# Kernel tuning notes

Measured on AMD Instinct MI355X. Metric: run time of the kernel, lower is better.

The kernel has to match this reference:

```python
import jax, jax.numpy as jnp
import numpy as np

B, S, D, H = 2, 4096, 256, 8
P = 64               # proj_dim_l
R = S // P           # proj_dim_r = 64, P*R == S
DH = D // H          # head_dim = 32


def setup_inputs() -> dict:
    key = jax.random.key(0)
    kx, kl, kr, kv, ko = jax.random.split(key, 5)
    scale = 0.05  # stand-in for xavier-uniform scale
    x  = jax.random.normal(kx, (B, S, D), dtype=jnp.float32)
    Wl = jax.random.normal(kl, (D, P), dtype=jnp.float32) * scale
    Wr = jax.random.normal(kr, (D, R), dtype=jnp.float32) * scale
    Wv = jax.random.normal(kv, (D, D), dtype=jnp.float32) * scale
    Wo = jax.random.normal(ko, (D, D), dtype=jnp.float32) * scale
    return {"x": x, "Wl": Wl, "Wr": Wr, "Wv": Wv, "Wo": Wo}


def reference(x, Wl, Wr, Wv, Wo):
    b, s, d = x.shape
    # value projection + head split -> (b, H, S, DH). Dropout p=0 (eval) = identity.
    v = (x @ Wv).reshape(b, s, H, DH).transpose(0, 2, 1, 3)
    # factorized score: row n is vec(outer(l_n, r_n)) of length P*R == S
    l = x @ Wl                                   # (b, S, P)
    r = x @ Wr                                   # (b, S, R)
    attn = (l[:, :, :, None] * r[:, :, None, :]).reshape(b, s, s)  # (b, S, S)
    score = jax.nn.softmax(attn, axis=-1)        # (b, S, S)
    # shared score across heads, per-head value matmul
    o = jnp.einsum('bnm,bhmd->bhnd', score, v)   # (b, H, S, DH)
    o = o.transpose(0, 2, 1, 3).reshape(b, s, d) # concat heads
    return o @ Wo
```

## Files before the change

### kernel.cpp

```cpp
#include <hip/hip_runtime.h>
#include <hip/hip_bf16.h>

typedef __attribute__((ext_vector_type(8))) __bf16 bf16x8;
typedef __attribute__((ext_vector_type(4))) __bf16 bf16x4;
typedef __attribute__((ext_vector_type(4))) float  f32x4;

#define MFMA16(a, b, c) __builtin_amdgcn_mfma_f32_16x16x32_bf16((a), (b), (c), 0, 0, 0)

static constexpr size_t OFF_WVT  = 0;
static constexpr size_t OFF_WLT  = OFF_WVT + 256 * 256 * 2;
static constexpr size_t OFF_WRT  = OFF_WLT + 64 * 256 * 2;
static constexpr size_t OFF_WOT  = OFF_WRT + 64 * 256 * 2;
static constexpr size_t OFF_VT   = 1u << 20;
static constexpr size_t OFF_L    = 6u << 20;
static constexpr size_t OFF_R    = 8u << 20;
static constexpr size_t OFF_PART = 10u << 20;
static constexpr size_t OFF_ZP   = 26u << 20;

__device__ __forceinline__ float fast_exp2(float x) {
  float e;
  asm("v_exp_f32 %0, %1" : "=v"(e) : "v"(x));
  return e;
}

__device__ __forceinline__ bf16x8 cvt8(float4 a, float4 b) {
  bf16x8 o;
  o[0] = (__bf16)a.x; o[1] = (__bf16)a.y; o[2] = (__bf16)a.z; o[3] = (__bf16)a.w;
  o[4] = (__bf16)b.x; o[5] = (__bf16)b.y; o[6] = (__bf16)b.z; o[7] = (__bf16)b.w;
  return o;
}

__global__ __launch_bounds__(256) void k_prepw(const float* __restrict__ Wv,
                                               const float* __restrict__ Wl,
                                               const float* __restrict__ Wr,
                                               const float* __restrict__ Wo,
                                               __bf16* __restrict__ Wvt,
                                               __bf16* __restrict__ Wlt,
                                               __bf16* __restrict__ Wrt,
                                               __bf16* __restrict__ Wot) {
  const int idx = blockIdx.x * 256 + threadIdx.x;
  if (idx < 65536) {
    const int k = idx >> 8, n = idx & 255;
    Wvt[n * 256 + k] = (__bf16)Wv[idx];
  } else if (idx < 81920) {
    const int j = idx - 65536;
    const int k = j >> 6, n = j & 63;
    Wlt[n * 256 + k] = (__bf16)Wl[j];
  } else if (idx < 98304) {
    const int j = idx - 81920;
    const int k = j >> 6, n = j & 63;
    Wrt[n * 256 + k] = (__bf16)Wr[j];
  } else {
    const int j = idx - 98304;
    const int k = j >> 8, n = j & 255;
    Wot[n * 256 + k] = (__bf16)Wo[j];
  }
}

__global__ __launch_bounds__(256) void k_proj(const float* __restrict__ x,
                                              const __bf16* __restrict__ Wvt,
                                              const __bf16* __restrict__ Wlt,
                                              const __bf16* __restrict__ Wrt,
                                              __bf16* __restrict__ Vt,
                                              float* __restrict__ lbuf,
                                              float* __restrict__ rbuf) {
  __shared__ __align__(16) __bf16 vs[8 * 64 * 8];
  const int t = threadIdx.x;
  const int lane = t & 63, wave = t >> 6;
  const int l16 = lane & 15, quad = lane >> 4;
  const int wr = wave >> 1, wc = wave & 1;
  const int rbk = blockIdx.x;
  const int ct  = blockIdx.y;
  const __bf16* Wt;
  int colbase;
  if (ct < 4)       { Wt = Wvt; colbase = ct * 64; }
  else if (ct == 4) { Wt = Wlt; colbase = 0; }
  else              { Wt = Wrt; colbase = 0; }
  const int row0 = rbk * 64 + wr * 32;
  const int c0   = colbase + wc * 32;
  f32x4 acc[2][2] = {};
  for (int kk = 0; kk < 256; kk += 32) {
    const int ko = kk + quad * 8;
    const float* xr0 = x + (size_t)(row0 + l16) * 256 + ko;
    const float* xr1 = x + (size_t)(row0 + 16 + l16) * 256 + ko;
    bf16x8 a0 = cvt8(*(const float4*)xr0, *(const float4*)(xr0 + 4));
    bf16x8 a1 = cvt8(*(const float4*)xr1, *(const float4*)(xr1 + 4));
    bf16x8 b0 = *(const bf16x8*)(Wt + (size_t)(c0 + l16) * 256 + ko);
    bf16x8 b1 = *(const bf16x8*)(Wt + (size_t)(c0 + 16 + l16) * 256 + ko);
    acc[0][0] = MFMA16(a0, b0, acc[0][0]);
    acc[0][1] = MFMA16(a0, b1, acc[0][1]);
    acc[1][0] = MFMA16(a1, b0, acc[1][0]);
    acc[1][1] = MFMA16(a1, b1, acc[1][1]);
  }
  if (ct < 4) {
#pragma unroll
    for (int mt = 0; mt < 2; ++mt)
#pragma unroll
      for (int nt = 0; nt < 2; ++nt) {
        const int m8 = wr * 4 + mt * 2 + (quad >> 1);
        const int d  = wc * 32 + nt * 16 + l16;
        bf16x4 o;
        o.x = (__bf16)acc[mt][nt][0];
        o.y = (__bf16)acc[mt][nt][1];
        o.z = (__bf16)acc[mt][nt][2];
        o.w = (__bf16)acc[mt][nt][3];
        *(bf16x4*)(&vs[m8 * 512 + d * 8 + (quad & 1) * 4]) = o;
      }
    __syncthreads();
    const int m8 = t >> 5, s32 = t & 31;
    const int bat = rbk >> 6, mc = rbk & 63;
    bf16x8 a = *(const bf16x8*)(&vs[m8 * 512 + s32 * 16]);
    bf16x8 b = *(const bf16x8*)(&vs[m8 * 512 + s32 * 16 + 8]);
    __bf16* dst = Vt + (size_t)bat * 1048576 + (size_t)mc * 16384 +
                  m8 * 2048 + ct * 512 + s32 * 16;
    *(bf16x8*)dst       = a;
    *(bf16x8*)(dst + 8) = b;
  } else {
    float* dstb = (ct == 4) ? lbuf : rbuf;
#pragma unroll
    for (int mt = 0; mt < 2; ++mt)
#pragma unroll
      for (int nt = 0; nt < 2; ++nt) {
        const int col = c0 + nt * 16 + l16;
        const int gr  = rbk * 64 + wr * 32 + mt * 16 + quad * 4;
#pragma unroll
        for (int rr = 0; rr < 4; ++rr)
          dstb[(size_t)(gr + rr) * 64 + col] = acc[mt][nt][rr];
      }
  }
}

__global__ __launch_bounds__(512, 2) void k_attn(const float* __restrict__ lbuf,
                                                 const float* __restrict__ rbuf,
                                                 const __bf16* __restrict__ Vt,
                                                 __bf16* __restrict__ part,
                                                 float* __restrict__ zpart) {
  __shared__ __align__(16) char smem[74240];
  __bf16* vt0 = (__bf16*)smem;
  __bf16* vt1 = (__bf16*)(smem + 32768);
  float*  ls  = (float*)(smem + 65536);
  const int t = threadIdx.x;
  const int lane = t & 63, w = t >> 6;
  const int l16 = lane & 15, quad = lane >> 4;
  const int wr = w >> 1, wc = w & 1;
  const int rb = blockIdx.x;
  const int sp = blockIdx.y;
  const int g0 = rb * 128;
  const int bat = rb >> 5;
  const __bf16* Vbase = Vt + (size_t)bat * 1048576;
  const int ck0 = sp * 16;

  {
    const int idx = t * 4;
    const int row = idx >> 4, c = idx & 15;
    f32x4 v = *(const f32x4*)(lbuf + (size_t)(g0 + row) * 64 + ck0 + c);
    ls[row * 17 + c + 0] = v[0];
    ls[row * 17 + c + 1] = v[1];
    ls[row * 17 + c + 2] = v[2];
    ls[row * 17 + c + 3] = v[3];
  }
  const float LOG2E = 1.44269504088896f;
  float rreg[2][16];
#pragma unroll
  for (int mt = 0; mt < 2; ++mt) {
    const float* rp = rbuf + (size_t)(g0 + wr * 32 + mt * 16 + l16) * 64;
    f32x4 a = *(const f32x4*)(rp + quad * 8);
    f32x4 b = *(const f32x4*)(rp + quad * 8 + 4);
    f32x4 c = *(const f32x4*)(rp + 32 + quad * 8);
    f32x4 d = *(const f32x4*)(rp + 32 + quad * 8 + 4);
#pragma unroll
    for (int j = 0; j < 4; ++j) {
      rreg[mt][j]      = a[j] * LOG2E;
      rreg[mt][4 + j]  = b[j] * LOG2E;
      rreg[mt][8 + j]  = c[j] * LOG2E;
      rreg[mt][12 + j] = d[j] * LOG2E;
    }
  }

  f32x4 acc[2][8] = {};
  float zacc[2] = {0.f, 0.f};
  bf16x8 stg[4];

  {
    const __bf16* src = Vbase + (size_t)ck0 * 16384;
#pragma unroll
    for (int i = 0; i < 4; ++i) stg[i] = *(const bf16x8*)(src + (size_t)(i * 512 + t) * 8);
#pragma unroll
    for (int i = 0; i < 4; ++i) *(bf16x8*)(vt0 + (i * 512 + t) * 8) = stg[i];
  }
  __syncthreads();

  for (int kc = 0; kc < 16; ++kc) {
    __bf16* cur = (kc & 1) ? vt1 : vt0;
    __bf16* nxt = (kc & 1) ? vt0 : vt1;
    if (kc < 15) {
      const __bf16* src = Vbase + (size_t)(ck0 + kc + 1) * 16384;
#pragma unroll
      for (int i = 0; i < 4; ++i) stg[i] = *(const bf16x8*)(src + (size_t)(i * 512 + t) * 8);
    }
    bf16x8 af[2][2];
#pragma unroll
    for (int mt = 0; mt < 2; ++mt) {
      const float lv = ls[(wr * 32 + mt * 16 + l16) * 17 + kc];
#pragma unroll
      for (int kk = 0; kk < 2; ++kk)
#pragma unroll
        for (int j = 0; j < 8; ++j) {
          const float e = fast_exp2(lv * rreg[mt][kk * 8 + j]);
          zacc[mt] += e;
          af[mt][kk][j] = (__bf16)e;
        }
    }
#pragma unroll
    for (int kk = 0; kk < 2; ++kk)
#pragma unroll
      for (int nt = 0; nt < 8; ++nt) {
        bf16x8 bv = *(const bf16x8*)(cur + (kk * 4 + quad) * 2048 +
                                     (wc * 128 + nt * 16 + l16) * 8);
        acc[0][nt] = MFMA16(af[0][kk], bv, acc[0][nt]);
        acc[1][nt] = MFMA16(af[1][kk], bv, acc[1][nt]);
      }
    if (kc < 15) {
#pragma unroll
      for (int i = 0; i < 4; ++i) *(bf16x8*)(nxt + (i * 512 + t) * 8) = stg[i];
    }
    __syncthreads();
  }

#pragma unroll
  for (int mt = 0; mt < 2; ++mt) {
    float z = zacc[mt];
    z += __shfl_xor(z, 16);
    z += __shfl_xor(z, 32);
    if (wc == 0 && quad == 0)
      zpart[(size_t)sp * 8192 + g0 + wr * 32 + mt * 16 + l16] = z;
  }

  __bf16* ctile = (__bf16*)smem;
#pragma unroll
  for (int mt = 0; mt < 2; ++mt)
#pragma unroll
    for (int nt = 0; nt < 8; ++nt) {
      const int r0 = wr * 32 + mt * 16 + quad * 4;
      const int c  = wc * 128 + nt * 16 + l16;
#pragma unroll
      for (int rr = 0; rr < 4; ++rr)
        ctile[(r0 + rr) * 264 + c] = (__bf16)acc[mt][nt][rr];
    }
  __syncthreads();
  __bf16* pb = part + (size_t)sp * (8192 * 256);
#pragma unroll
  for (int p = 0; p < 8; ++p) {
    const int u = p * 512 + t;
    const int row = u >> 5, seg = u & 31;
    *(bf16x8*)(pb + (size_t)(g0 + row) * 256 + seg * 8) =
        *(const bf16x8*)(ctile + row * 264 + seg * 8);
  }
}

__global__ __launch_bounds__(256) void k_outfix(const __bf16* __restrict__ part,
                                                const float* __restrict__ zpart,
                                                const __bf16* __restrict__ Wot,
                                                float* __restrict__ out) {
  const int t = threadIdx.x;
  const int lane = t & 63, w = t >> 6;
  const int l16 = lane & 15, quad = lane >> 4;
  const int wr = w >> 1, wc = w & 1;
  const int rb = blockIdx.x;
  const int arow = rb * 32 + wr * 16 + l16;
  float z = 0.f;
#pragma unroll
  for (int s = 0; s < 4; ++s) z += zpart[(size_t)s * 8192 + arow];
  const float iz = 1.0f / z;
  f32x4 acc[8] = {};
#pragma unroll 2
  for (int ks = 0; ks < 8; ++ks) {
    const int k0 = ks * 32 + quad * 8;
    float sum[8] = {};
#pragma unroll
    for (int s = 0; s < 4; ++s) {
      bf16x8 p = *(const bf16x8*)(part + (size_t)s * (8192 * 256) + (size_t)arow * 256 + k0);
#pragma unroll
      for (int j = 0; j < 8; ++j) sum[j] += (float)p[j];
    }
    bf16x8 afr;
#pragma unroll
    for (int j = 0; j < 8; ++j) afr[j] = (__bf16)(sum[j] * iz);
#pragma unroll
    for (int nt = 0; nt < 8; ++nt) {
      bf16x8 bv = *(const bf16x8*)(Wot + (size_t)(wc * 128 + nt * 16 + l16) * 256 + k0);
      acc[nt] = MFMA16(afr, bv, acc[nt]);
    }
  }
#pragma unroll
  for (int nt = 0; nt < 8; ++nt) {
    const int col = wc * 128 + nt * 16 + l16;
    const int r0  = rb * 32 + wr * 16 + quad * 4;
#pragma unroll
    for (int rr = 0; rr < 4; ++rr)
      out[(size_t)(r0 + rr) * 256 + col] = acc[nt][rr];
  }
}

extern "C" void kernel_launch(void* const* d_in, const int* in_sizes, int n_in,
                              void* d_out, int out_size, void* d_ws, size_t ws_size,
                              hipStream_t stream) {
  const float* x  = (const float*)d_in[0];
  const float* Wl = (const float*)d_in[1];
  const float* Wr = (const float*)d_in[2];
  const float* Wv = (const float*)d_in[3];
  const float* Wo = (const float*)d_in[4];
  char* ws = (char*)d_ws;
  __bf16* Wvt = (__bf16*)(ws + OFF_WVT);
  __bf16* Wlt = (__bf16*)(ws + OFF_WLT);
  __bf16* Wrt = (__bf16*)(ws + OFF_WRT);
  __bf16* Wot = (__bf16*)(ws + OFF_WOT);
  __bf16* Vt  = (__bf16*)(ws + OFF_VT);
  float*  lb  = (float*)(ws + OFF_L);
  float*  rbf = (float*)(ws + OFF_R);
  __bf16* prt = (__bf16*)(ws + OFF_PART);
  float*  zp  = (float*)(ws + OFF_ZP);
  float*  out = (float*)d_out;

  k_prepw<<<640, 256, 0, stream>>>(Wv, Wl, Wr, Wo, Wvt, Wlt, Wrt, Wot);
  k_proj<<<dim3(128, 6), 256, 0, stream>>>(x, Wvt, Wlt, Wrt, Vt, lb, rbf);
  k_attn<<<dim3(64, 4), 512, 0, stream>>>(lb, rbf, Vt, prt, zp);
  k_outfix<<<256, 256, 0, stream>>>(prt, zp, Wot, out);
}
```

Baseline: 136.2 us.

## Fuse weight prep into projection kernel and retile attention waves to 2x4

Removes the separate weight-conversion kernel. Each projection block now converts its own weight slice from fp32 into a transposed bf16 tile in shared memory, and the Wo transpose is spread across the l/r projection blocks. The attention kernel's wave layout changes from 4x2 to 2x4, so each wave handles 64 rows by 64 columns and every V fragment read from LDS feeds four MFMAs instead of two. This saves one launch and some global traffic, at the cost of redundant weight conversion in every block and higher register pressure in the attention kernel.

```diff
diff --git a/kernel.cpp b/kernel.cpp
--- a/kernel.cpp
+++ b/kernel.cpp
@@ -7,10 +7,7 @@
 
 #define MFMA16(a, b, c) __builtin_amdgcn_mfma_f32_16x16x32_bf16((a), (b), (c), 0, 0, 0)
 
-static constexpr size_t OFF_WVT  = 0;
-static constexpr size_t OFF_WLT  = OFF_WVT + 256 * 256 * 2;
-static constexpr size_t OFF_WRT  = OFF_WLT + 64 * 256 * 2;
-static constexpr size_t OFF_WOT  = OFF_WRT + 64 * 256 * 2;
+static constexpr size_t OFF_WOT  = 0;
 static constexpr size_t OFF_VT   = 1u << 20;
 static constexpr size_t OFF_L    = 6u << 20;
 static constexpr size_t OFF_R    = 8u << 20;
@@ -30,40 +27,16 @@
   return o;
 }
 
-__global__ __launch_bounds__(256) void k_prepw(const float* __restrict__ Wv,
-                                               const float* __restrict__ Wl,
-                                               const float* __restrict__ Wr,
-                                               const float* __restrict__ Wo,
-                                               __bf16* __restrict__ Wvt,
-                                               __bf16* __restrict__ Wlt,
-                                               __bf16* __restrict__ Wrt,
-                                               __bf16* __restrict__ Wot) {
-  const int idx = blockIdx.x * 256 + threadIdx.x;
-  if (idx < 65536) {
-    const int k = idx >> 8, n = idx & 255;
-    Wvt[n * 256 + k] = (__bf16)Wv[idx];
-  } else if (idx < 81920) {
-    const int j = idx - 65536;
-    const int k = j >> 6, n = j & 63;
-    Wlt[n * 256 + k] = (__bf16)Wl[j];
-  } else if (idx < 98304) {
-    const int j = idx - 81920;
-    const int k = j >> 6, n = j & 63;
-    Wrt[n * 256 + k] = (__bf16)Wr[j];
-  } else {
-    const int j = idx - 98304;
-    const int k = j >> 8, n = j & 255;
-    Wot[n * 256 + k] = (__bf16)Wo[j];
-  }
-}
-
 __global__ __launch_bounds__(256) void k_proj(const float* __restrict__ x,
-                                              const __bf16* __restrict__ Wvt,
-                                              const __bf16* __restrict__ Wlt,
-                                              const __bf16* __restrict__ Wrt,
+                                              const float* __restrict__ Wv,
+                                              const float* __restrict__ Wl,
+                                              const float* __restrict__ Wr,
+                                              const float* __restrict__ Wo,
                                               __bf16* __restrict__ Vt,
                                               float* __restrict__ lbuf,
-                                              float* __restrict__ rbuf) {
+                                              float* __restrict__ rbuf,
+                                              __bf16* __restrict__ Wot) {
+  __shared__ __align__(16) __bf16 wt[64 * 264];
   __shared__ __align__(16) __bf16 vs[8 * 64 * 8];
   const int t = threadIdx.x;
   const int lane = t & 63, wave = t >> 6;
@@ -71,13 +44,35 @@
   const int wr = wave >> 1, wc = wave & 1;
   const int rbk = blockIdx.x;
   const int ct  = blockIdx.y;
-  const __bf16* Wt;
-  int colbase;
-  if (ct < 4)       { Wt = Wvt; colbase = ct * 64; }
-  else if (ct == 4) { Wt = Wlt; colbase = 0; }
-  else              { Wt = Wrt; colbase = 0; }
+  const float* Wsrc;
+  int wstride, colbase;
+  if (ct < 4)       { Wsrc = Wv; wstride = 256; colbase = ct * 64; }
+  else if (ct == 4) { Wsrc = Wl; wstride = 64;  colbase = 0; }
+  else              { Wsrc = Wr; wstride = 64;  colbase = 0; }
+
+  if (ct >= 4) {
+    const int j = ((ct - 4) * 128 + rbk) * 256 + t;
+    const int k = j >> 8, n = j & 255;
+    Wot[n * 256 + k] = (__bf16)Wo[j];
+  }
+
+  {
+    const int kr = t >> 4;
+    const int n4 = (t & 15) * 4;
+#pragma unroll
+    for (int kk = 0; kk < 16; ++kk) {
+      const int k = kk * 16 + kr;
+      float4 v = *(const float4*)(Wsrc + (size_t)k * wstride + colbase + n4);
+      wt[(n4 + 0) * 264 + k] = (__bf16)v.x;
+      wt[(n4 + 1) * 264 + k] = (__bf16)v.y;
+      wt[(n4 + 2) * 264 + k] = (__bf16)v.z;
+      wt[(n4 + 3) * 264 + k] = (__bf16)v.w;
+    }
+  }
+  __syncthreads();
+
   const int row0 = rbk * 64 + wr * 32;
-  const int c0   = colbase + wc * 32;
+  const int c0l  = wc * 32;
   f32x4 acc[2][2] = {};
   for (int kk = 0; kk < 256; kk += 32) {
     const int ko = kk + quad * 8;
@@ -85,8 +80,8 @@
     const float* xr1 = x + (size_t)(row0 + 16 + l16) * 256 + ko;
     bf16x8 a0 = cvt8(*(const float4*)xr0, *(const float4*)(xr0 + 4));
     bf16x8 a1 = cvt8(*(const float4*)xr1, *(const float4*)(xr1 + 4));
-    bf16x8 b0 = *(const bf16x8*)(Wt + (size_t)(c0 + l16) * 256 + ko);
-    bf16x8 b1 = *(const bf16x8*)(Wt + (size_t)(c0 + 16 + l16) * 256 + ko);
+    bf16x8 b0 = *(const bf16x8*)(wt + (c0l + l16) * 264 + ko);
+    bf16x8 b1 = *(const bf16x8*)(wt + (c0l + 16 + l16) * 264 + ko);
     acc[0][0] = MFMA16(a0, b0, acc[0][0]);
     acc[0][1] = MFMA16(a0, b1, acc[0][1]);
     acc[1][0] = MFMA16(a1, b0, acc[1][0]);
@@ -121,7 +116,7 @@
     for (int mt = 0; mt < 2; ++mt)
 #pragma unroll
       for (int nt = 0; nt < 2; ++nt) {
-        const int col = c0 + nt * 16 + l16;
+        const int col = c0l + nt * 16 + l16;
         const int gr  = rbk * 64 + wr * 32 + mt * 16 + quad * 4;
 #pragma unroll
         for (int rr = 0; rr < 4; ++rr)
@@ -142,7 +137,7 @@
   const int t = threadIdx.x;
   const int lane = t & 63, w = t >> 6;
   const int l16 = lane & 15, quad = lane >> 4;
-  const int wr = w >> 1, wc = w & 1;
+  const int wr = w >> 2, wc = w & 3;
   const int rb = blockIdx.x;
   const int sp = blockIdx.y;
   const int g0 = rb * 128;
@@ -160,10 +155,10 @@
     ls[row * 17 + c + 3] = v[3];
   }
   const float LOG2E = 1.44269504088896f;
-  float rreg[2][16];
-#pragma unroll
-  for (int mt = 0; mt < 2; ++mt) {
-    const float* rp = rbuf + (size_t)(g0 + wr * 32 + mt * 16 + l16) * 64;
+  float rreg[4][16];
+#pragma unroll
+  for (int mt = 0; mt < 4; ++mt) {
+    const float* rp = rbuf + (size_t)(g0 + wr * 64 + mt * 16 + l16) * 64;
     f32x4 a = *(const f32x4*)(rp + quad * 8);
     f32x4 b = *(const f32x4*)(rp + quad * 8 + 4);
     f32x4 c = *(const f32x4*)(rp + 32 + quad * 8);
@@ -177,8 +172,8 @@
     }
   }
 
-  f32x4 acc[2][8] = {};
-  float zacc[2] = {0.f, 0.f};
+  f32x4 acc[4][4] = {};
+  float zacc[4] = {0.f, 0.f, 0.f, 0.f};
   bf16x8 stg[4];
 
   {
@@ -198,10 +193,10 @@
 #pragma unroll
       for (int i = 0; i < 4; ++i) stg[i] = *(const bf16x8*)(src + (size_t)(i * 512 + t) * 8);
     }
-    bf16x8 af[2][2];
-#pragma unroll
-    for (int mt = 0; mt < 2; ++mt) {
-      const float lv = ls[(wr * 32 + mt * 16 + l16) * 17 + kc];
+    bf16x8 af[4][2];
+#pragma unroll
+    for (int mt = 0; mt < 4; ++mt) {
+      const float lv = ls[(wr * 64 + mt * 16 + l16) * 17 + kc];
 #pragma unroll
       for (int kk = 0; kk < 2; ++kk)
 #pragma unroll
@@ -214,11 +209,13 @@
 #pragma unroll
     for (int kk = 0; kk < 2; ++kk)
 #pragma unroll
-      for (int nt = 0; nt < 8; ++nt) {
+      for (int nt = 0; nt < 4; ++nt) {
         bf16x8 bv = *(const bf16x8*)(cur + (kk * 4 + quad) * 2048 +
-                                     (wc * 128 + nt * 16 + l16) * 8);
+                                     (wc * 64 + nt * 16 + l16) * 8);
         acc[0][nt] = MFMA16(af[0][kk], bv, acc[0][nt]);
         acc[1][nt] = MFMA16(af[1][kk], bv, acc[1][nt]);
+        acc[2][nt] = MFMA16(af[2][kk], bv, acc[2][nt]);
+        acc[3][nt] = MFMA16(af[3][kk], bv, acc[3][nt]);
       }
     if (kc < 15) {
 #pragma unroll
@@ -228,21 +225,21 @@
   }
 
 #pragma unroll
-  for (int mt = 0; mt < 2; ++mt) {
+  for (int mt = 0; mt < 4; ++mt) {
     float z = zacc[mt];
     z += __shfl_xor(z, 16);
     z += __shfl_xor(z, 32);
     if (wc == 0 && quad == 0)
-      zpart[(size_t)sp * 8192 + g0 + wr * 32 + mt * 16 + l16] = z;
+      zpart[(size_t)sp * 8192 + g0 + wr * 64 + mt * 16 + l16] = z;
   }
 
   __bf16* ctile = (__bf16*)smem;
 #pragma unroll
-  for (int mt = 0; mt < 2; ++mt)
-#pragma unroll
-    for (int nt = 0; nt < 8; ++nt) {
-      const int r0 = wr * 32 + mt * 16 + quad * 4;
-      const int c  = wc * 128 + nt * 16 + l16;
+  for (int mt = 0; mt < 4; ++mt)
+#pragma unroll
+    for (int nt = 0; nt < 4; ++nt) {
+      const int r0 = wr * 64 + mt * 16 + quad * 4;
+      const int c  = wc * 64 + nt * 16 + l16;
 #pragma unroll
       for (int rr = 0; rr < 4; ++rr)
         ctile[(r0 + rr) * 264 + c] = (__bf16)acc[mt][nt][rr];
@@ -311,9 +308,6 @@
   const float* Wv = (const float*)d_in[3];
   const float* Wo = (const float*)d_in[4];
   char* ws = (char*)d_ws;
-  __bf16* Wvt = (__bf16*)(ws + OFF_WVT);
-  __bf16* Wlt = (__bf16*)(ws + OFF_WLT);
-  __bf16* Wrt = (__bf16*)(ws + OFF_WRT);
   __bf16* Wot = (__bf16*)(ws + OFF_WOT);
   __bf16* Vt  = (__bf16*)(ws + OFF_VT);
   float*  lb  = (float*)(ws + OFF_L);
@@ -322,8 +316,7 @@
   float*  zp  = (float*)(ws + OFF_ZP);
   float*  out = (float*)d_out;
 
-  k_prepw<<<640, 256, 0, stream>>>(Wv, Wl, Wr, Wo, Wvt, Wlt, Wrt, Wot);
-  k_proj<<<dim3(128, 6), 256, 0, stream>>>(x, Wvt, Wlt, Wrt, Vt, lb, rbf);
+  k_proj<<<dim3(128, 6), 256, 0, stream>>>(x, Wv, Wl, Wr, Wo, Vt, lb, rbf, Wot);
   k_attn<<<dim3(64, 4), 512, 0, stream>>>(lb, rbf, Vt, prt, zp);
   k_outfix<<<256, 256, 0, stream>>>(prt, zp, Wot, out);
 }
```

New measurement: 137.1 us. Within noise of the previous version (+0.7%).
